# Optimization experiments

Hardware: AMD Instinct MI355X
Metric: run time of the kernel (lower is better)

Reference implementation:

```python
import jax, jax.numpy as jnp
import numpy as np

B, S, D, H = 4, 2048, 1024, 16
HD = D // H  # head_dim = 64
SCALE = HD ** -0.5


def setup_inputs() -> dict:
    key = jax.random.key(0)
    ks = jax.random.split(key, 6)
    x = jax.random.normal(ks[0], (B, S, D), dtype=jnp.float32)
    attn_bias = jax.random.normal(ks[1], (H, S, S), dtype=jnp.float32)
    std = D ** -0.5
    qkv_w = jax.random.normal(ks[2], (3 * D, D), dtype=jnp.float32) * std
    qkv_b = jnp.zeros((3 * D,), dtype=jnp.float32)
    out_w = jax.random.normal(ks[3], (D, D), dtype=jnp.float32) * std
    out_b = jnp.zeros((D,), dtype=jnp.float32)
    return {"x": x, "attn_bias": attn_bias, "qkv_w": qkv_w, "qkv_b": qkv_b,
            "out_w": out_w, "out_b": out_b}


def reference(x, attn_bias, qkv_w, qkv_b, out_w, out_b):
    # qkv projection: (B,S,3D) -> (3,B,H,S,hd)
    qkv = (jnp.einsum('bsd,ed->bse', x, qkv_w) + qkv_b)
    qkv = qkv.reshape(B, S, 3, H, HD).transpose(2, 0, 3, 1, 4)
    q, k, v = qkv[0], qkv[1], qkv[2]
    # scores (B,H,S,S) with learned additive bias
    attn = jnp.einsum('bhqd,bhkd->bhqk', q, k) * SCALE + attn_bias[None]
    attn = jax.nn.softmax(attn, axis=-1)  # dropout p=0.0 -> identity
    out = jnp.einsum('bhqk,bhkd->bhqd', attn, v)
    out = out.transpose(0, 2, 1, 3).reshape(B, S, D)
    return jnp.einsum('bsd,ed->bse', out, out_w) + out_b
```

## Files before the change

### kernel.cpp

```cpp
#include <hip/hip_runtime.h>
#include <hip/hip_bf16.h>

#define B_ 4
#define S_ 2048
#define D_ 1024
#define H_ 16
#define HD_ 64

typedef __attribute__((ext_vector_type(8))) short short8;
typedef __attribute__((ext_vector_type(4))) short short4v;
typedef __attribute__((ext_vector_type(4))) float f32x4;

__device__ inline short f2bf(float f) {
    union { __hip_bfloat16 h; short s; } u;
    u.h = __float2bfloat16(f);
    return u.s;
}

__device__ inline void gload_lds16(const void* g, void* l) {
    __builtin_amdgcn_global_load_lds(
        (const __attribute__((address_space(1))) void*)g,
        (__attribute__((address_space(3))) void*)l, 16, 0, 0);
}

__global__ void cast_f32_bf16(const float* __restrict__ in, short* __restrict__ out, int n4) {
    int idx = blockIdx.x * blockDim.x + threadIdx.x;
    int stride = gridDim.x * blockDim.x;
    for (int i = idx; i < n4; i += stride) {
        float4 v = reinterpret_cast<const float4*>(in)[i];
        short4v o;
        o[0] = f2bf(v.x); o[1] = f2bf(v.y); o[2] = f2bf(v.z); o[3] = f2bf(v.w);
        reinterpret_cast<short4v*>(out)[i] = o;
    }
}

template<int EPI>
__global__ __launch_bounds__(256) void gemm_bt(
    const short* __restrict__ A, const short* __restrict__ Bm,
    const float* __restrict__ bias, int M, int N, int K,
    short* __restrict__ qo, short* __restrict__ ko, short* __restrict__ vo,
    float* __restrict__ co)
{
    __shared__ __attribute__((aligned(16))) short As[128 * 64];
    __shared__ __attribute__((aligned(16))) short Bs[128 * 64];

    const int t = threadIdx.x;
    const int wid = t >> 6, l = t & 63;
    const int wm = wid >> 1, wn = wid & 1;
    const int m0 = blockIdx.y * 128, n0 = blockIdx.x * 128;
    const int lr = l & 15, lg = l >> 4;

    f32x4 acc[4][4] = {};

    const int rowA = t >> 3;
    const int col8 = (t & 7) << 3;

    for (int k0 = 0; k0 < K; k0 += 64) {
#pragma unroll
        for (int c = 0; c < 4; ++c) {
            gload_lds16(A + (size_t)(m0 + c * 32 + rowA) * K + k0 + col8, &As[c * 2048 + t * 8]);
            gload_lds16(Bm + (size_t)(n0 + c * 32 + rowA) * K + k0 + col8, &Bs[c * 2048 + t * 8]);
        }
        __syncthreads();
#pragma unroll
        for (int kk = 0; kk < 2; ++kk) {
            short8 af[4], bfr[4];
#pragma unroll
            for (int i = 0; i < 4; ++i)
                af[i] = *(const short8*)&As[(wm * 64 + i * 16 + lr) * 64 + kk * 32 + lg * 8];
#pragma unroll
            for (int j = 0; j < 4; ++j)
                bfr[j] = *(const short8*)&Bs[(wn * 64 + j * 16 + lr) * 64 + kk * 32 + lg * 8];
#pragma unroll
            for (int i = 0; i < 4; ++i)
#pragma unroll
                for (int j = 0; j < 4; ++j)
                    acc[i][j] = __builtin_amdgcn_mfma_f32_16x16x32_bf16(af[i], bfr[j], acc[i][j], 0, 0, 0);
        }
        __syncthreads();
    }

#pragma unroll
    for (int i = 0; i < 4; ++i) {
#pragma unroll
        for (int j = 0; j < 4; ++j) {
#pragma unroll
            for (int r = 0; r < 4; ++r) {
                int gm = m0 + wm * 64 + i * 16 + lg * 4 + r;
                int gn = n0 + wn * 64 + j * 16 + lr;
                float v = acc[i][j][r] + bias[gn];
                if (EPI == 0) {
                    int which = gn >> 10, h = (gn >> 6) & 15, hd = gn & 63;
                    int b = gm >> 11, s = gm & 2047;
                    short bv = f2bf(v);
                    if (which == 0)      qo[((size_t)(b * H_ + h) * S_ + s) * HD_ + hd] = bv;
                    else if (which == 1) ko[((size_t)(b * H_ + h) * S_ + s) * HD_ + hd] = bv;
                    else                 vo[((size_t)(b * H_ + h) * HD_ + hd) * S_ + s] = bv;
                } else {
                    co[(size_t)gm * N + gn] = v;
                }
            }
        }
    }
}

__global__ __launch_bounds__(256) void attn_kernel(
    const short* __restrict__ qb, const short* __restrict__ kb,
    const short* __restrict__ vtb, const float* __restrict__ bias,
    short* __restrict__ ab)
{
    __shared__ __attribute__((aligned(16))) short Ks[128 * 72];
    __shared__ __attribute__((aligned(16))) short Vts[64 * 136];
    __shared__ __attribute__((aligned(16))) short Pl[4 * 32 * 136];

    const int t = threadIdx.x, wid = t >> 6, l = t & 63;
    const int lr = l & 15, lg = l >> 4;
    const int q0 = blockIdx.x * 128;
    const int h = blockIdx.y >> 2, b = blockIdx.y & 3;
    const int bh = b * H_ + h;

    const short* Qbase = qb + (size_t)bh * S_ * HD_;
    const short* Kbase = kb + (size_t)bh * S_ * HD_;
    const short* Vbase = vtb + (size_t)bh * HD_ * S_;
    const float* biasH = bias + (size_t)h * S_ * S_;

    short8 qf[2][2];
#pragma unroll
    for (int i = 0; i < 2; ++i)
#pragma unroll
        for (int kk = 0; kk < 2; ++kk)
            qf[i][kk] = *(const short8*)(Qbase + (size_t)(q0 + wid * 32 + i * 16 + lr) * HD_ + kk * 32 + lg * 8);

    f32x4 o[2][4] = {};
    float m_run[2][4], l_run[2][4];
#pragma unroll
    for (int i = 0; i < 2; ++i)
#pragma unroll
        for (int r = 0; r < 4; ++r) { m_run[i][r] = -1e30f; l_run[i][r] = 0.f; }

    const int krow = t >> 3, kcol = (t & 7) << 3;
    const int vrow = t >> 4, vcol = (t & 15) << 3;

    for (int kv0 = 0; kv0 < S_; kv0 += 128) {
        short8 kreg[4], vreg[4];
#pragma unroll
        for (int c = 0; c < 4; ++c) {
            kreg[c] = *(const short8*)(Kbase + (size_t)(kv0 + c * 32 + krow) * HD_ + kcol);
            vreg[c] = *(const short8*)(Vbase + (size_t)(c * 16 + vrow) * S_ + kv0 + vcol);
        }
#pragma unroll
        for (int c = 0; c < 4; ++c) {
            *(short8*)&Ks[(c * 32 + krow) * 72 + kcol] = kreg[c];
            *(short8*)&Vts[(c * 16 + vrow) * 136 + vcol] = vreg[c];
        }
        __syncthreads();

        f32x4 sc[2][8];
#pragma unroll
        for (int j = 0; j < 8; ++j) {
            short8 kf0 = *(const short8*)&Ks[(j * 16 + lr) * 72 + lg * 8];
            short8 kf1 = *(const short8*)&Ks[(j * 16 + lr) * 72 + 32 + lg * 8];
#pragma unroll
            for (int i = 0; i < 2; ++i) {
                f32x4 z = {};
                z = __builtin_amdgcn_mfma_f32_16x16x32_bf16(qf[i][0], kf0, z, 0, 0, 0);
                sc[i][j] = __builtin_amdgcn_mfma_f32_16x16x32_bf16(qf[i][1], kf1, z, 0, 0, 0);
            }
        }

#pragma unroll
        for (int i = 0; i < 2; ++i) {
#pragma unroll
            for (int r = 0; r < 4; ++r) {
                int qrow = q0 + wid * 32 + i * 16 + lg * 4 + r;
                const float* brow = biasH + (size_t)qrow * S_ + kv0 + lr;
                float vj[8];
                float mx = -1e30f;
#pragma unroll
                for (int j = 0; j < 8; ++j) {
                    float v = sc[i][j][r] * 0.125f + brow[j * 16];
                    vj[j] = v;
                    mx = fmaxf(mx, v);
                }
#pragma unroll
                for (int d = 1; d < 16; d <<= 1)
                    mx = fmaxf(mx, __shfl_xor(mx, d));
                float mnew = fmaxf(m_run[i][r], mx);
                float fi = __expf(m_run[i][r] - mnew);
                m_run[i][r] = mnew;
                l_run[i][r] *= fi;
#pragma unroll
                for (int nf = 0; nf < 4; ++nf) o[i][nf][r] *= fi;
                float ls = 0.f;
#pragma unroll
                for (int j = 0; j < 8; ++j) {
                    float p = __expf(vj[j] - mnew);
                    ls += p;
                    Pl[wid * 4352 + (i * 16 + lg * 4 + r) * 136 + j * 16 + lr] = f2bf(p);
                }
                l_run[i][r] += ls;
            }
        }
        __syncthreads();

#pragma unroll
        for (int kk = 0; kk < 4; ++kk) {
            short8 pa[2], vb[4];
#pragma unroll
            for (int i = 0; i < 2; ++i)
                pa[i] = *(const short8*)&Pl[wid * 4352 + (i * 16 + lr) * 136 + kk * 32 + lg * 8];
#pragma unroll
            for (int nf = 0; nf < 4; ++nf)
                vb[nf] = *(const short8*)&Vts[(nf * 16 + lr) * 136 + kk * 32 + lg * 8];
#pragma unroll
            for (int i = 0; i < 2; ++i)
#pragma unroll
                for (int nf = 0; nf < 4; ++nf)
                    o[i][nf] = __builtin_amdgcn_mfma_f32_16x16x32_bf16(pa[i], vb[nf], o[i][nf], 0, 0, 0);
        }
        __syncthreads();
    }

#pragma unroll
    for (int i = 0; i < 2; ++i) {
#pragma unroll
        for (int r = 0; r < 4; ++r) {
            float ls = l_run[i][r];
#pragma unroll
            for (int d = 1; d < 16; d <<= 1) ls += __shfl_xor(ls, d);
            float inv = 1.f / ls;
            int qrow = q0 + wid * 32 + i * 16 + lg * 4 + r;
#pragma unroll
            for (int nf = 0; nf < 4; ++nf)
                ab[((size_t)b * S_ + qrow) * D_ + h * HD_ + nf * 16 + lr] = f2bf(o[i][nf][r] * inv);
        }
    }
}

extern "C" void kernel_launch(void* const* d_in, const int* in_sizes, int n_in,
                              void* d_out, int out_size, void* d_ws, size_t ws_size,
                              hipStream_t stream) {
    (void)in_sizes; (void)n_in; (void)out_size; (void)ws_size;
    const float* x     = (const float*)d_in[0];
    const float* bias  = (const float*)d_in[1];
    const float* qkv_w = (const float*)d_in[2];
    const float* qkv_b = (const float*)d_in[3];
    const float* out_w = (const float*)d_in[4];
    const float* out_b = (const float*)d_in[5];
    float* out = (float*)d_out;

    char* w = (char*)d_ws;
    short* xb    = (short*)(w + 0);
    short* wqkvb = (short*)(w + (16u << 20));
    short* woutb = (short*)(w + (22u << 20));
    short* qb    = (short*)(w + (24u << 20));
    short* kb    = (short*)(w + (40u << 20));
    short* vtb   = (short*)(w + (56u << 20));
    short* ab    = (short*)(w + (72u << 20));

    cast_f32_bf16<<<2048, 256, 0, stream>>>(x, xb, (B_ * S_ * D_) / 4);
    cast_f32_bf16<<<1024, 256, 0, stream>>>(qkv_w, wqkvb, (3 * D_ * D_) / 4);
    cast_f32_bf16<<<512, 256, 0, stream>>>(out_w, woutb, (D_ * D_) / 4);

    dim3 g1(24, 64);
    gemm_bt<0><<<g1, 256, 0, stream>>>(xb, wqkvb, qkv_b, B_ * S_, 3 * D_, D_,
                                       qb, kb, vtb, nullptr);

    dim3 ga(16, B_ * H_);
    attn_kernel<<<ga, 256, 0, stream>>>(qb, kb, vtb, bias, ab);

    dim3 g2(8, 64);
    gemm_bt<1><<<g2, 256, 0, stream>>>(ab, woutb, out_b, B_ * S_, D_, D_,
                                       nullptr, nullptr, nullptr, out);
}
```

Measured before the change: 753.0 us.

## Store V row-major, transpose in LDS, prefetch 64-wide KV tiles

The QKV GEMM epilogue now writes V in the same row-major head layout as Q and K. Previously V was scattered with a stride of the sequence length. The attention kernel shrinks its KV tile from 128 to 64 keys and prefetches the next K/V tile into registers while the current one is computed. V is transposed into LDS with scalar stores. It also drops the barrier between the softmax and PV stages, since P is private to each wave, and adds an occupancy hint to the launch bounds. The scalar transposed LDS stores and more loop iterations add overhead and possible bank conflicts, in exchange for lower LDS use and better latency hiding.

```diff
diff --git a/kernel.cpp b/kernel.cpp
--- a/kernel.cpp
+++ b/kernel.cpp
@@ -93,9 +93,10 @@
                     int which = gn >> 10, h = (gn >> 6) & 15, hd = gn & 63;
                     int b = gm >> 11, s = gm & 2047;
                     short bv = f2bf(v);
-                    if (which == 0)      qo[((size_t)(b * H_ + h) * S_ + s) * HD_ + hd] = bv;
-                    else if (which == 1) ko[((size_t)(b * H_ + h) * S_ + s) * HD_ + hd] = bv;
-                    else                 vo[((size_t)(b * H_ + h) * HD_ + hd) * S_ + s] = bv;
+                    size_t idx = ((size_t)(b * H_ + h) * S_ + s) * HD_ + hd;
+                    if (which == 0)      qo[idx] = bv;
+                    else if (which == 1) ko[idx] = bv;
+                    else                 vo[idx] = bv;
                 } else {
                     co[(size_t)gm * N + gn] = v;
                 }
@@ -104,14 +105,14 @@
     }
 }
 
-__global__ __launch_bounds__(256) void attn_kernel(
+__global__ __launch_bounds__(256, 4) void attn_kernel(
     const short* __restrict__ qb, const short* __restrict__ kb,
-    const short* __restrict__ vtb, const float* __restrict__ bias,
+    const short* __restrict__ vb_, const float* __restrict__ bias,
     short* __restrict__ ab)
 {
-    __shared__ __attribute__((aligned(16))) short Ks[128 * 72];
-    __shared__ __attribute__((aligned(16))) short Vts[64 * 136];
-    __shared__ __attribute__((aligned(16))) short Pl[4 * 32 * 136];
+    __shared__ __attribute__((aligned(16))) short Ks[64 * 72];
+    __shared__ __attribute__((aligned(16))) short Vts[64 * 72];
+    __shared__ __attribute__((aligned(16))) short Pl[4 * 32 * 72];
 
     const int t = threadIdx.x, wid = t >> 6, l = t & 63;
     const int lr = l & 15, lg = l >> 4;
@@ -121,7 +122,7 @@
 
     const short* Qbase = qb + (size_t)bh * S_ * HD_;
     const short* Kbase = kb + (size_t)bh * S_ * HD_;
-    const short* Vbase = vtb + (size_t)bh * HD_ * S_;
+    const short* Vbase = vb_ + (size_t)bh * S_ * HD_;
     const float* biasH = bias + (size_t)h * S_ * S_;
 
     short8 qf[2][2];
@@ -138,26 +139,39 @@
 #pragma unroll
         for (int r = 0; r < 4; ++r) { m_run[i][r] = -1e30f; l_run[i][r] = 0.f; }
 
-    const int krow = t >> 3, kcol = (t & 7) << 3;
-    const int vrow = t >> 4, vcol = (t & 15) << 3;
-
-    for (int kv0 = 0; kv0 < S_; kv0 += 128) {
-        short8 kreg[4], vreg[4];
-#pragma unroll
-        for (int c = 0; c < 4; ++c) {
-            kreg[c] = *(const short8*)(Kbase + (size_t)(kv0 + c * 32 + krow) * HD_ + kcol);
-            vreg[c] = *(const short8*)(Vbase + (size_t)(c * 16 + vrow) * S_ + kv0 + vcol);
-        }
-#pragma unroll
-        for (int c = 0; c < 4; ++c) {
-            *(short8*)&Ks[(c * 32 + krow) * 72 + kcol] = kreg[c];
-            *(short8*)&Vts[(c * 16 + vrow) * 136 + vcol] = vreg[c];
-        }
-        __syncthreads();
-
-        f32x4 sc[2][8];
-#pragma unroll
-        for (int j = 0; j < 8; ++j) {
+    const int srow = t >> 3;
+    const int scol = (t & 7) << 3;
+
+    short8 kreg[2], vreg[2];
+#pragma unroll
+    for (int c = 0; c < 2; ++c) {
+        kreg[c] = *(const short8*)(Kbase + (size_t)(c * 32 + srow) * HD_ + scol);
+        vreg[c] = *(const short8*)(Vbase + (size_t)(c * 32 + srow) * HD_ + scol);
+    }
+
+    for (int t0 = 0; t0 < 32; ++t0) {
+        const int kv0 = t0 * 64;
+#pragma unroll
+        for (int c = 0; c < 2; ++c) {
+            *(short8*)&Ks[(c * 32 + srow) * 72 + scol] = kreg[c];
+#pragma unroll
+            for (int e = 0; e < 8; ++e)
+                Vts[(scol + e) * 72 + c * 32 + srow] = vreg[c][e];
+        }
+        __syncthreads();
+
+        if (t0 < 31) {
+            const int kvn = kv0 + 64;
+#pragma unroll
+            for (int c = 0; c < 2; ++c) {
+                kreg[c] = *(const short8*)(Kbase + (size_t)(kvn + c * 32 + srow) * HD_ + scol);
+                vreg[c] = *(const short8*)(Vbase + (size_t)(kvn + c * 32 + srow) * HD_ + scol);
+            }
+        }
+
+        f32x4 sc[2][4];
+#pragma unroll
+        for (int j = 0; j < 4; ++j) {
             short8 kf0 = *(const short8*)&Ks[(j * 16 + lr) * 72 + lg * 8];
             short8 kf1 = *(const short8*)&Ks[(j * 16 + lr) * 72 + 32 + lg * 8];
 #pragma unroll
@@ -174,10 +188,10 @@
             for (int r = 0; r < 4; ++r) {
                 int qrow = q0 + wid * 32 + i * 16 + lg * 4 + r;
                 const float* brow = biasH + (size_t)qrow * S_ + kv0 + lr;
-                float vj[8];
+                float vj[4];
                 float mx = -1e30f;
 #pragma unroll
-                for (int j = 0; j < 8; ++j) {
+                for (int j = 0; j < 4; ++j) {
                     float v = sc[i][j][r] * 0.125f + brow[j * 16];
                     vj[j] = v;
                     mx = fmaxf(mx, v);
@@ -193,25 +207,24 @@
                 for (int nf = 0; nf < 4; ++nf) o[i][nf][r] *= fi;
                 float ls = 0.f;
 #pragma unroll
-                for (int j = 0; j < 8; ++j) {
+                for (int j = 0; j < 4; ++j) {
                     float p = __expf(vj[j] - mnew);
                     ls += p;
-                    Pl[wid * 4352 + (i * 16 + lg * 4 + r) * 136 + j * 16 + lr] = f2bf(p);
+                    Pl[wid * 2304 + (i * 16 + lg * 4 + r) * 72 + j * 16 + lr] = f2bf(p);
                 }
                 l_run[i][r] += ls;
             }
         }
-        __syncthreads();
-
-#pragma unroll
-        for (int kk = 0; kk < 4; ++kk) {
+
+#pragma unroll
+        for (int kk = 0; kk < 2; ++kk) {
             short8 pa[2], vb[4];
 #pragma unroll
             for (int i = 0; i < 2; ++i)
-                pa[i] = *(const short8*)&Pl[wid * 4352 + (i * 16 + lr) * 136 + kk * 32 + lg * 8];
+                pa[i] = *(const short8*)&Pl[wid * 2304 + (i * 16 + lr) * 72 + kk * 32 + lg * 8];
 #pragma unroll
             for (int nf = 0; nf < 4; ++nf)
-                vb[nf] = *(const short8*)&Vts[(nf * 16 + lr) * 136 + kk * 32 + lg * 8];
+                vb[nf] = *(const short8*)&Vts[(nf * 16 + lr) * 72 + kk * 32 + lg * 8];
 #pragma unroll
             for (int i = 0; i < 2; ++i)
 #pragma unroll
@@ -255,7 +268,7 @@
     short* woutb = (short*)(w + (22u << 20));
     short* qb    = (short*)(w + (24u << 20));
     short* kb    = (short*)(w + (40u << 20));
-    short* vtb   = (short*)(w + (56u << 20));
+    short* vb    = (short*)(w + (56u << 20));
     short* ab    = (short*)(w + (72u << 20));
 
     cast_f32_bf16<<<2048, 256, 0, stream>>>(x, xb, (B_ * S_ * D_) / 4);
@@ -264,10 +277,10 @@
 
     dim3 g1(24, 64);
     gemm_bt<0><<<g1, 256, 0, stream>>>(xb, wqkvb, qkv_b, B_ * S_, 3 * D_, D_,
-                                       qb, kb, vtb, nullptr);
+                                       qb, kb, vb, nullptr);
 
     dim3 ga(16, B_ * H_);
-    attn_kernel<<<ga, 256, 0, stream>>>(qb, kb, vtb, bias, ab);
+    attn_kernel<<<ga, 256, 0, stream>>>(qb, kb, vb, bias, ab);
 
     dim3 g2(8, 64);
     gemm_bt<1><<<g2, 256, 0, stream>>>(ab, woutb, out_b, B_ * S_, D_, D_,
```

New measurement: 951.3 us. +26.3%, slower.
